# Performance work log

Measured on AMD Instinct MI355X. Metric: run time of the kernel, lower is better.

The kernel has to match this reference:

```python
import jax, jax.numpy as jnp
import numpy as np

DIM = 384
HEADS = 6
HEAD_DIM = 64
WIN = 14
SCALE = HEAD_DIM ** -0.5
EPS = 1e-5  # torch LayerNorm default


def setup_inputs() -> dict:
    key = jax.random.key(0)
    ks = jax.random.split(key, 8)
    w = lambda k, shape: jax.random.normal(k, shape, dtype=jnp.float32) * 0.02
    return {
        "x": jax.random.normal(ks[0], (1, 336, 336, DIM), dtype=jnp.float32),
        "qkv_w": w(ks[1], (DIM, 3 * DIM)),
        "qkv_b": jnp.zeros((3 * DIM,), jnp.float32),
        "proj_w": w(ks[2], (DIM, DIM)),
        "proj_b": jnp.zeros((DIM,), jnp.float32),
        "rel_pos_h": w(ks[3], (2 * WIN - 1, HEAD_DIM)),
        "rel_pos_w": w(ks[4], (2 * WIN - 1, HEAD_DIM)),
        "norm1_w": jnp.ones((DIM,), jnp.float32),
        "norm1_b": jnp.zeros((DIM,), jnp.float32),
        "norm2_w": jnp.ones((DIM,), jnp.float32),
        "norm2_b": jnp.zeros((DIM,), jnp.float32),
        "fc1_w": w(ks[5], (DIM, 4 * DIM)),
        "fc1_b": jnp.zeros((4 * DIM,), jnp.float32),
        "fc2_w": w(ks[6], (4 * DIM, DIM)),
        "fc2_b": jnp.zeros((DIM,), jnp.float32),
    }


def _layernorm(x, w, b):
    m = jnp.mean(x, axis=-1, keepdims=True)
    v = jnp.var(x, axis=-1, keepdims=True)
    return (x - m) / jnp.sqrt(v + EPS) * w + b


def _rel_table(rel_pos):
    coords = np.arange(WIN)[:, None] - np.arange(WIN)[None, :] + (WIN - 1)
    return rel_pos[coords]


def _block(x, qkv_w, qkv_b, proj_w, proj_b, rel_pos_h, rel_pos_w,
           norm1_w, norm1_b, norm2_w, norm2_b, fc1_w, fc1_b, fc2_w, fc2_b):
    B, H, W, C = x.shape
    shortcut = x
    x = _layernorm(x, norm1_w, norm1_b)

    nH, nW = H // WIN, W // WIN
    xw = x.reshape(B, nH, WIN, nW, WIN, C).transpose(0, 1, 3, 2, 4, 5)
    xw = xw.reshape(B * nH * nW, WIN * WIN, C)  # [Nw, 196, C]
    Nw, L = xw.shape[0], WIN * WIN

    # --- attention with decomposed rel-pos ---
    qkv = xw @ qkv_w + qkv_b                         # [Nw, 196, 3C]
    qkv = qkv.reshape(Nw, L, 3, HEADS, HEAD_DIM).transpose(2, 0, 3, 1, 4)
    q, k, v = qkv[0], qkv[1], qkv[2]                 # [Nw, h, 196, d]

    attn = jnp.einsum("bhqd,bhkd->bhqk", q * SCALE, k)  # [Nw, h, 196, 196]

    Rh = _rel_table(rel_pos_h)                       # [14, 14, d]
    Rw = _rel_table(rel_pos_w)
    r_q = q.reshape(Nw, HEADS, WIN, WIN, HEAD_DIM)
    rel_h = jnp.einsum("bnhwc,hkc->bnhwk", r_q, Rh)  # [Nw, h, 14, 14, 14]
    rel_w = jnp.einsum("bnhwc,wkc->bnhwk", r_q, Rw)
    attn = (attn.reshape(Nw, HEADS, WIN, WIN, WIN, WIN)
            + rel_h[..., :, None] + rel_w[..., None, :]).reshape(Nw, HEADS, L, L)

    attn = jax.nn.softmax(attn, axis=-1)
    out = jnp.einsum("bhqk,bhkd->bhqd", attn, v)     # [Nw, h, 196, d]
    out = out.transpose(0, 2, 1, 3).reshape(Nw, L, C)
    out = out @ proj_w + proj_b

    # --- window unpartition ---
    out = out.reshape(B, nH, nW, WIN, WIN, C).transpose(0, 1, 3, 2, 4, 5)
    out = out.reshape(B, H, W, C)

    x = shortcut + out
    h = _layernorm(x, norm2_w, norm2_b)
    h = jax.nn.gelu(h @ fc1_w + fc1_b, approximate=False) @ fc2_w + fc2_b
    return x + h


def reference(x, qkv_w, qkv_b, proj_w, proj_b, rel_pos_h, rel_pos_w,
              norm1_w, norm1_b, norm2_w, norm2_b, fc1_w, fc1_b, fc2_w, fc2_b):
    return _block(x, qkv_w, qkv_b, proj_w, proj_b, rel_pos_h, rel_pos_w,
                  norm1_w, norm1_b, norm2_w, norm2_b, fc1_w, fc1_b, fc2_w, fc2_b)
```

## Files before the change

kernel.cpp:

```cpp
#include <hip/hip_runtime.h>
#include <math.h>

#define TOKENS 112896
#define C      384
#define NQKV   1152
#define NFC    1536
#define HEADS  6
#define HD     64
#define WIN    14
#define L      196
#define NWS    24
#define SCALEF 0.125f

typedef unsigned int  u32;
typedef unsigned short u16;
typedef short short8 __attribute__((ext_vector_type(8)));
typedef float floatx4 __attribute__((ext_vector_type(4)));

__device__ __forceinline__ u16 f2bf(float f) {
  u32 u = __float_as_uint(f);
  u += 0x7FFFu + ((u >> 16) & 1u);
  return (u16)(u >> 16);
}

__device__ __forceinline__ float bf2f(u16 v) {
  return __uint_as_float((u32)v << 16);
}

__device__ __forceinline__ float gelu_f(float v) {
  float z = fabsf(v) * 0.70710678118654752f;
  float t = 1.0f / (1.0f + 0.3275911f * z);
  float poly = t * (0.254829592f + t * (-0.284496736f + t * (1.421413741f +
               t * (-1.453152027f + t * 1.061405429f))));
  float erfv = 1.0f - poly * __expf(-z * z);
  erfv = copysignf(erfv, v);
  return 0.5f * v * (1.0f + erfv);
}

__device__ __forceinline__ void async16(u16* lds, const u16* g) {
  __builtin_amdgcn_global_load_lds((const __attribute__((address_space(1))) void*)g,
                                   (__attribute__((address_space(3))) void*)lds,
                                   16, 0, 0);
}

__device__ __forceinline__ int win_to_tok(int r) {
  int n = r / L, l = r % L;
  int wh = n / NWS, ww = n % NWS;
  int ih = l / WIN, iw = l % WIN;
  return (wh * WIN + ih) * 336 + ww * WIN + iw;
}

__global__ __launch_bounds__(256) void conv_t_kernel(const float* __restrict__ in,
    u16* __restrict__ out, int K, int N)
{
  __shared__ u16 tile[32][33];
  const int kb = blockIdx.y * 32, nb = blockIdx.x * 32;
  const int tx = threadIdx.x & 31, ty = threadIdx.x >> 5;
#pragma unroll
  for (int i = 0; i < 4; i++) {
    int k = kb + ty + i * 8;
    tile[ty + i * 8][tx] = f2bf(in[(size_t)k * N + nb + tx]);
  }
  __syncthreads();
#pragma unroll
  for (int i = 0; i < 4; i++) {
    int n = nb + ty + i * 8;
    out[(size_t)n * K + kb + tx] = tile[tx][ty + i * 8];
  }
}

template<bool PERMUTE>
__global__ __launch_bounds__(128) void ln_kernel(const float* __restrict__ x,
    const float* __restrict__ w, const float* __restrict__ b,
    u16* __restrict__ out)
{
  const int t = blockIdx.x;
  const int tid = threadIdx.x;
  const float* xr = x + (size_t)t * C;
  float v0 = xr[tid], v1 = xr[tid + 128], v2 = xr[tid + 256];
  float s  = v0 + v1 + v2;
  float ss = v0 * v0 + v1 * v1 + v2 * v2;
#pragma unroll
  for (int off = 32; off > 0; off >>= 1) {
    s  += __shfl_down(s, off);
    ss += __shfl_down(ss, off);
  }
  __shared__ float red[4];
  if ((tid & 63) == 0) { red[(tid >> 6) * 2 + 0] = s; red[(tid >> 6) * 2 + 1] = ss; }
  __syncthreads();
  float S  = red[0] + red[2];
  float SS = red[1] + red[3];
  float mean = S * (1.0f / C);
  float var  = SS * (1.0f / C) - mean * mean;
  float rstd = rsqrtf(var + 1e-5f);
  size_t orow;
  if (PERMUTE) {
    int h_ = t / 336, w_ = t % 336;
    int wh = h_ / WIN, ih = h_ % WIN;
    int ww = w_ / WIN, iw = w_ % WIN;
    orow = (size_t)((wh * NWS + ww) * L + ih * WIN + iw);
  } else {
    orow = (size_t)t;
  }
  u16* op = out + orow * C;
  op[tid]       = f2bf((v0 - mean) * rstd * w[tid]       + b[tid]);
  op[tid + 128] = f2bf((v1 - mean) * rstd * w[tid + 128] + b[tid + 128]);
  op[tid + 256] = f2bf((v2 - mean) * rstd * w[tid + 256] + b[tid + 256]);
}

template<int MODE>
__global__ __launch_bounds__(256, 4) void gemm_bf16(
    const u16* __restrict__ A, const u16* __restrict__ Bt,
    const float* __restrict__ bias, const float* __restrict__ res,
    void* __restrict__ outv, int N, int K)
{
  __shared__ u16 As[2][128 * 32];
  __shared__ u16 Bs[2][128 * 32];
  const int tid = threadIdx.x;
  const int w = tid >> 6, l = tid & 63;

  const int nwg = gridDim.x * gridDim.y;
  int lin = blockIdx.y * gridDim.x + blockIdx.x;
  {
    int q8 = nwg >> 3, r8 = nwg & 7;
    int xcd = lin & 7, sub = lin >> 3;
    lin = (xcd < r8 ? xcd * (q8 + 1) : r8 * (q8 + 1) + (xcd - r8) * q8) + sub;
  }
  const int bx = lin % gridDim.x, by = lin / gridDim.x;
  const int bm = by * 128, bn = bx * 128;

  const int wm = (w >> 1) * 64, wn = (w & 1) * 64;
  const int lm = l & 15, quad = l >> 4;

  floatx4 acc[4][4] = {};

  const u16* Asrc[2]; const u16* Bsrc[2];
#pragma unroll
  for (int q = 0; q < 2; q++) {
    int t = q * 256 + tid;
    int r = t >> 2, gl = t & 3;
    int sg = gl ^ ((r >> 1) & 3);
    Asrc[q] = A  + (size_t)(bm + r) * K + sg * 8;
    Bsrc[q] = Bt + (size_t)(bn + r) * K + sg * 8;
  }
  u16* Ad[2]; u16* Bd[2];
#pragma unroll
  for (int q = 0; q < 2; q++) {
    Ad[q] = &As[0][(q * 256 + w * 64) * 8];
    Bd[q] = &Bs[0][(q * 256 + w * 64) * 8];
  }
  const int bufoff = 128 * 32;

  auto stage = [&](int buf, int kt) {
#pragma unroll
    for (int q = 0; q < 2; q++) {
      async16(Ad[q] + buf * bufoff, Asrc[q] + kt);
      async16(Bd[q] + buf * bufoff, Bsrc[q] + kt);
    }
  };

  const int xg = (quad ^ ((lm >> 1) & 3)) * 8;
  const u16* ard[4]; const u16* brd[4];
#pragma unroll
  for (int i = 0; i < 4; i++) {
    ard[i] = &As[0][(wm + i * 16 + lm) * 32 + xg];
    brd[i] = &Bs[0][(wn + i * 16 + lm) * 32 + xg];
  }

  const int nk = K >> 5;
  stage(0, 0);
  __syncthreads();

  for (int t = 0; t < nk; t++) {
    const int buf = t & 1;
    if (t + 1 < nk) stage(buf ^ 1, (t + 1) << 5);
    const int bo = buf * bufoff;
    short8 bfr[4];
#pragma unroll
    for (int j = 0; j < 4; j++) bfr[j] = *(const short8*)(brd[j] + bo);
#pragma unroll
    for (int i = 0; i < 4; i++) {
      short8 afr = *(const short8*)(ard[i] + bo);
#pragma unroll
      for (int j = 0; j < 4; j++)
        acc[i][j] = __builtin_amdgcn_mfma_f32_16x16x32_bf16(afr, bfr[j], acc[i][j], 0, 0, 0);
    }
    __syncthreads();
  }

  const int colbase = bn + wn + lm;
  float bb[4];
#pragma unroll
  for (int j = 0; j < 4; j++) bb[j] = bias[colbase + j * 16];

#pragma unroll
  for (int i = 0; i < 4; i++) {
#pragma unroll
    for (int reg = 0; reg < 4; reg++) {
      int row = bm + wm + i * 16 + quad * 4 + reg;
      size_t ro;
      if (MODE == 1) ro = (size_t)win_to_tok(row) * N;
      else           ro = (size_t)row * N;
#pragma unroll
      for (int j = 0; j < 4; j++) {
        float v = acc[i][j][reg] + bb[j];
        int col = colbase + j * 16;
        if (MODE == 0) {
          ((u16*)outv)[ro + col] = f2bf(v);
        } else if (MODE == 1) {
          ((float*)outv)[ro + col] = v + res[ro + col];
        } else if (MODE == 2) {
          ((u16*)outv)[ro + col] = f2bf(gelu_f(v));
        } else {
          ((float*)outv)[ro + col] = v + res[ro + col];
        }
      }
    }
  }
}

__global__ __launch_bounds__(256, 2) void attn_kernel(
    const u16* __restrict__ qkv,
    const float* __restrict__ relh, const float* __restrict__ relw,
    u16* __restrict__ out)
{
  __shared__ float Plds[4][512];
  __shared__ u16 rhlds[208 * 28];
  __shared__ u16 rwlds[208 * 28];
  __shared__ u16 Klds[32 * 64];
  __shared__ u16 Vtl[64 * 40];

  const int n = blockIdx.x / HEADS;
  const int h = blockIdx.x % HEADS;
  const int tid = threadIdx.x;
  const int w = tid >> 6;
  const int l = tid & 63;
  const int lm = l & 15;
  const int quad = l >> 4;
  const size_t base = (size_t)n * L;

  short8 qf[4][2];
#pragma unroll
  for (int i = 0; i < 4; i++) {
    int rt = w + 4 * i;
    if (rt <= 12) {
      int row = rt * 16 + lm; if (row > 195) row = 195;
      const u16* qp = qkv + (base + row) * NQKV + h * HD + quad * 8;
#pragma unroll
      for (int kf = 0; kf < 2; kf++)
        qf[i][kf] = *(const short8*)(qp + kf * 32);
    }
  }

  {
    short8 tf[2][2][2];
#pragma unroll
    for (int tab = 0; tab < 2; tab++) {
      const float* tp = tab ? relw : relh;
#pragma unroll
      for (int ct = 0; ct < 2; ct++) {
        int t = ct * 16 + lm;
#pragma unroll
        for (int kf = 0; kf < 2; kf++) {
          short8 v = {0, 0, 0, 0, 0, 0, 0, 0};
          if (t < 27) {
            const float* p = tp + t * HD + kf * 32 + quad * 8;
            float4 a = *(const float4*)p;
            float4 b = *(const float4*)(p + 4);
            v[0] = (short)f2bf(a.x); v[1] = (short)f2bf(a.y);
            v[2] = (short)f2bf(a.z); v[3] = (short)f2bf(a.w);
            v[4] = (short)f2bf(b.x); v[5] = (short)f2bf(b.y);
            v[6] = (short)f2bf(b.z); v[7] = (short)f2bf(b.w);
          }
          tf[tab][ct][kf] = v;
        }
      }
    }
#pragma unroll
    for (int i = 0; i < 4; i++) {
      int rt = w + 4 * i;
      if (rt > 12) continue;
#pragma unroll
      for (int tab = 0; tab < 2; tab++) {
        u16* dst = tab ? rwlds : rhlds;
#pragma unroll
        for (int ct = 0; ct < 2; ct++) {
          floatx4 acc = {};
          acc = __builtin_amdgcn_mfma_f32_16x16x32_bf16(qf[i][0], tf[tab][ct][0], acc, 0, 0, 0);
          acc = __builtin_amdgcn_mfma_f32_16x16x32_bf16(qf[i][1], tf[tab][ct][1], acc, 0, 0, 0);
          int t = ct * 16 + lm;
          if (t < 28) {
#pragma unroll
            for (int reg = 0; reg < 4; reg++) {
              int q = rt * 16 + quad * 4 + reg;
              dst[q * 28 + t] = f2bf(acc[reg]);
            }
          }
        }
      }
    }
  }

  floatx4 oacc[4][4] = {};
  float lsum[4][4] = {};

#pragma unroll 1
  for (int ks = 0; ks < 7; ks++) {
    __syncthreads();
    {
      int r = tid >> 3, g = tid & 7;
      int row = ks * 32 + r; if (row > 195) row = 195;
      uint4 kd = *(const uint4*)(qkv + (base + row) * NQKV + C + h * HD + g * 8);
      *(uint4*)&Klds[r * 64 + ((g ^ (r & 7)) * 8)] = kd;
    }
    {
      int r = tid & 31, seg = tid >> 5;
      int row = ks * 32 + r; if (row > 195) row = 195;
      uint4 vd = *(const uint4*)(qkv + (base + row) * NQKV + 2 * C + h * HD + seg * 8);
      union { uint4 u; u16 s[8]; } vv; vv.u = vd;
#pragma unroll
      for (int j = 0; j < 8; j++) Vtl[(seg * 8 + j) * 40 + r] = vv.s[j];
    }
    __syncthreads();

    short8 kfr[2][2];
#pragma unroll
    for (int ct = 0; ct < 2; ct++) {
      int krow = ct * 16 + lm;
#pragma unroll
      for (int kf = 0; kf < 2; kf++)
        kfr[ct][kf] = *(const short8*)&Klds[krow * 64 + (((kf * 4 + quad) ^ (krow & 7)) * 8)];
    }
    short8 vfr[4];
#pragma unroll
    for (int dt = 0; dt < 4; dt++)
      vfr[dt] = *(const short8*)&Vtl[(dt * 16 + lm) * 40 + quad * 8];

#pragma unroll
    for (int i = 0; i < 4; i++) {
      int rt = w + 4 * i;
      if (rt > 12) continue;
      floatx4 sc[2] = {};
#pragma unroll
      for (int ct = 0; ct < 2; ct++) {
        sc[ct] = __builtin_amdgcn_mfma_f32_16x16x32_bf16(qf[i][0], kfr[ct][0], sc[ct], 0, 0, 0);
        sc[ct] = __builtin_amdgcn_mfma_f32_16x16x32_bf16(qf[i][1], kfr[ct][1], sc[ct], 0, 0, 0);
      }
      float* Pw = Plds[w];
#pragma unroll
      for (int ct = 0; ct < 2; ct++) {
        int k = ks * 32 + ct * 16 + lm;
        int kh = (k * 293) >> 12;
        int kw2 = k - kh * 14;
        bool kval = (k < 196);
#pragma unroll
        for (int reg = 0; reg < 4; reg++) {
          int q = rt * 16 + quad * 4 + reg;
          int qh = (q * 293) >> 12;
          int qw = q - qh * 14;
          int th = qh - kh + 13; th = th < 0 ? 0 : th;
          int tw = qw - kw2 + 13;
          float bh = bf2f(rhlds[q * 28 + th]);
          float bw = bf2f(rwlds[q * 28 + tw]);
          float s = sc[ct][reg] * SCALEF + bh + bw;
          float p = kval ? __expf(s) : 0.0f;
          lsum[i][reg] += p;
          int prow = quad * 4 + reg;
          int col = ct * 16 + lm;
          Pw[prow * 32 + (((col >> 2) ^ (prow & 7)) * 4) + (col & 3)] = p;
        }
      }
      floatx4 pa = *(const floatx4*)&Pw[lm * 32 + (((2 * quad) ^ (lm & 7)) * 4)];
      floatx4 pb = *(const floatx4*)&Pw[lm * 32 + (((2 * quad + 1) ^ (lm & 7)) * 4)];
      short8 pfr;
#pragma unroll
      for (int j = 0; j < 4; j++) {
        pfr[j]     = (short)f2bf(pa[j]);
        pfr[4 + j] = (short)f2bf(pb[j]);
      }
#pragma unroll
      for (int dt = 0; dt < 4; dt++)
        oacc[i][dt] = __builtin_amdgcn_mfma_f32_16x16x32_bf16(pfr, vfr[dt], oacc[i][dt], 0, 0, 0);
    }
  }

#pragma unroll
  for (int i = 0; i < 4; i++) {
    int rt = w + 4 * i;
    if (rt > 12) continue;
#pragma unroll
    for (int reg = 0; reg < 4; reg++) {
      float v = lsum[i][reg];
      v += __shfl_xor(v, 1);
      v += __shfl_xor(v, 2);
      v += __shfl_xor(v, 4);
      v += __shfl_xor(v, 8);
      float inv = 1.0f / v;
      int row = rt * 16 + quad * 4 + reg;
      if (row < 196) {
        u16* op = out + (base + row) * C + h * HD + lm;
#pragma unroll
        for (int dt = 0; dt < 4; dt++) op[dt * 16] = f2bf(oacc[i][dt][reg] * inv);
      }
    }
  }
}

extern "C" void kernel_launch(void* const* d_in, const int* in_sizes, int n_in,
                              void* d_out, int out_size, void* d_ws, size_t ws_size,
                              hipStream_t stream)
{
  const float* x      = (const float*)d_in[0];
  const float* qkv_w  = (const float*)d_in[1];
  const float* qkv_b  = (const float*)d_in[2];
  const float* proj_w = (const float*)d_in[3];
  const float* proj_b = (const float*)d_in[4];
  const float* rel_h  = (const float*)d_in[5];
  const float* rel_w  = (const float*)d_in[6];
  const float* n1w    = (const float*)d_in[7];
  const float* n1b    = (const float*)d_in[8];
  const float* n2w    = (const float*)d_in[9];
  const float* n2b    = (const float*)d_in[10];
  const float* fc1_w  = (const float*)d_in[11];
  const float* fc1_b  = (const float*)d_in[12];
  const float* fc2_w  = (const float*)d_in[13];
  const float* fc2_b  = (const float*)d_in[14];

  u16*  W0 = (u16*)d_ws;
  u16*  W1 = (u16*)((char*)d_ws + 86704128);
  float* W2 = (float*)((char*)d_ws + 86704128 + 346816512);
  u16*  WT = (u16*)((char*)d_ws + 86704128 + 346816512 + 173408256);
  u16* qkv_wT  = WT;
  u16* proj_wT = qkv_wT + 442368;
  u16* fc1_wT  = proj_wT + 147456;
  u16* fc2_wT  = fc1_wT + 589824;

  conv_t_kernel<<<dim3(NQKV / 32, C / 32), 256, 0, stream>>>(qkv_w, qkv_wT, C, NQKV);
  conv_t_kernel<<<dim3(C / 32, C / 32), 256, 0, stream>>>(proj_w, proj_wT, C, C);
  conv_t_kernel<<<dim3(NFC / 32, C / 32), 256, 0, stream>>>(fc1_w, fc1_wT, C, NFC);
  conv_t_kernel<<<dim3(C / 32, NFC / 32), 256, 0, stream>>>(fc2_w, fc2_wT, NFC, C);

  ln_kernel<true><<<TOKENS, 128, 0, stream>>>(x, n1w, n1b, W0);
  gemm_bf16<0><<<dim3(NQKV / 128, TOKENS / 128), 256, 0, stream>>>(
      W0, qkv_wT, qkv_b, nullptr, W1, NQKV, C);
  attn_kernel<<<576 * HEADS, 256, 0, stream>>>(W1, rel_h, rel_w, W0);
  gemm_bf16<1><<<dim3(C / 128, TOKENS / 128), 256, 0, stream>>>(
      W0, proj_wT, proj_b, x, W2, C, C);
  ln_kernel<false><<<TOKENS, 128, 0, stream>>>(W2, n2w, n2b, W0);
  gemm_bf16<2><<<dim3(NFC / 128, TOKENS / 128), 256, 0, stream>>>(
      W0, fc1_wT, fc1_b, nullptr, W1, NFC, C);
  gemm_bf16<3><<<dim3(C / 128, TOKENS / 128), 256, 0, stream>>>(
      W1, fc2_wT, fc2_b, W2, (float*)d_out, C, NFC);
}
```

Before: 1.386 ms.

## Transpose MFMA operands for vectorized epilogue stores and unroll GEMM k-loop by two

```diff
diff --git a/kernel.cpp b/kernel.cpp
--- a/kernel.cpp
+++ b/kernel.cpp
@@ -25,6 +25,12 @@
 
 __device__ __forceinline__ float bf2f(u16 v) {
   return __uint_as_float((u32)v << 16);
+}
+
+__device__ __forceinline__ u32 pk2bf(float lo, float hi) {
+  u32 r;
+  asm("v_cvt_pk_bf16_f32 %0, %1, %2" : "=v"(r) : "v"(lo), "v"(hi));
+  return r;
 }
 
 __device__ __forceinline__ float gelu_f(float v) {
@@ -134,14 +140,14 @@
 
   floatx4 acc[4][4] = {};
 
-  const u16* Asrc[2]; const u16* Bsrc[2];
+  u32 aofs[2], bofs[2];
 #pragma unroll
   for (int q = 0; q < 2; q++) {
     int t = q * 256 + tid;
     int r = t >> 2, gl = t & 3;
     int sg = gl ^ ((r >> 1) & 3);
-    Asrc[q] = A  + (size_t)(bm + r) * K + sg * 8;
-    Bsrc[q] = Bt + (size_t)(bn + r) * K + sg * 8;
+    aofs[q] = (u32)((bm + r) * K + sg * 8);
+    bofs[q] = (u32)((bn + r) * K + sg * 8);
   }
   u16* Ad[2]; u16* Bd[2];
 #pragma unroll
@@ -149,15 +155,17 @@
     Ad[q] = &As[0][(q * 256 + w * 64) * 8];
     Bd[q] = &Bs[0][(q * 256 + w * 64) * 8];
   }
-  const int bufoff = 128 * 32;
-
-  auto stage = [&](int buf, int kt) {
-#pragma unroll
-    for (int q = 0; q < 2; q++) {
-      async16(Ad[q] + buf * bufoff, Asrc[q] + kt);
-      async16(Bd[q] + buf * bufoff, Bsrc[q] + kt);
-    }
-  };
+
+#define STAGE(buf, kt)                                         \
+  {                                                            \
+    const u16* Ap = A  + (kt);                                 \
+    const u16* Bp = Bt + (kt);                                 \
+    _Pragma("unroll")                                          \
+    for (int q = 0; q < 2; q++) {                              \
+      async16(Ad[q] + (buf) * 4096, Ap + aofs[q]);             \
+      async16(Bd[q] + (buf) * 4096, Bp + bofs[q]);             \
+    }                                                          \
+  }
 
   const int xg = (quad ^ ((lm >> 1) & 3)) * 8;
   const u16* ard[4]; const u16* brd[4];
@@ -167,53 +175,66 @@
     brd[i] = &Bs[0][(wn + i * 16 + lm) * 32 + xg];
   }
 
+#define COMPUTE(BO)                                                         \
+  {                                                                         \
+    short8 bfr[4];                                                          \
+    _Pragma("unroll")                                                       \
+    for (int i2 = 0; i2 < 4; i2++)                                          \
+      bfr[i2] = *(const short8*)(brd[i2] + (BO));                           \
+    _Pragma("unroll")                                                       \
+    for (int j2 = 0; j2 < 4; j2++) {                                        \
+      short8 afr = *(const short8*)(ard[j2] + (BO));                        \
+      _Pragma("unroll")                                                     \
+      for (int i2 = 0; i2 < 4; i2++)                                        \
+        acc[i2][j2] = __builtin_amdgcn_mfma_f32_16x16x32_bf16(              \
+            bfr[i2], afr, acc[i2][j2], 0, 0, 0);                            \
+    }                                                                       \
+  }
+
   const int nk = K >> 5;
-  stage(0, 0);
+  STAGE(0, 0);
   __syncthreads();
 
-  for (int t = 0; t < nk; t++) {
-    const int buf = t & 1;
-    if (t + 1 < nk) stage(buf ^ 1, (t + 1) << 5);
-    const int bo = buf * bufoff;
-    short8 bfr[4];
-#pragma unroll
-    for (int j = 0; j < 4; j++) bfr[j] = *(const short8*)(brd[j] + bo);
+  for (int t = 0; t < nk; t += 2) {
+    STAGE(1, (t + 1) << 5);
+    COMPUTE(0);
+    __syncthreads();
+    if (t + 2 < nk) STAGE(0, (t + 2) << 5);
+    COMPUTE(4096);
+    __syncthreads();
+  }
+#undef STAGE
+#undef COMPUTE
+
+  float4 bb[4];
+#pragma unroll
+  for (int i = 0; i < 4; i++)
+    bb[i] = *(const float4*)&bias[bn + wn + i * 16 + quad * 4];
+
+#pragma unroll
+  for (int j = 0; j < 4; j++) {
+    int m = bm + wm + j * 16 + lm;
+    size_t ro;
+    if (MODE == 1) ro = (size_t)win_to_tok(m) * N;
+    else           ro = (size_t)m * N;
 #pragma unroll
     for (int i = 0; i < 4; i++) {
-      short8 afr = *(const short8*)(ard[i] + bo);
-#pragma unroll
-      for (int j = 0; j < 4; j++)
-        acc[i][j] = __builtin_amdgcn_mfma_f32_16x16x32_bf16(afr, bfr[j], acc[i][j], 0, 0, 0);
-    }
-    __syncthreads();
-  }
-
-  const int colbase = bn + wn + lm;
-  float bb[4];
-#pragma unroll
-  for (int j = 0; j < 4; j++) bb[j] = bias[colbase + j * 16];
-
-#pragma unroll
-  for (int i = 0; i < 4; i++) {
-#pragma unroll
-    for (int reg = 0; reg < 4; reg++) {
-      int row = bm + wm + i * 16 + quad * 4 + reg;
-      size_t ro;
-      if (MODE == 1) ro = (size_t)win_to_tok(row) * N;
-      else           ro = (size_t)row * N;
-#pragma unroll
-      for (int j = 0; j < 4; j++) {
-        float v = acc[i][j][reg] + bb[j];
-        int col = colbase + j * 16;
-        if (MODE == 0) {
-          ((u16*)outv)[ro + col] = f2bf(v);
-        } else if (MODE == 1) {
-          ((float*)outv)[ro + col] = v + res[ro + col];
-        } else if (MODE == 2) {
-          ((u16*)outv)[ro + col] = f2bf(gelu_f(v));
-        } else {
-          ((float*)outv)[ro + col] = v + res[ro + col];
-        }
+      int n0 = bn + wn + i * 16 + quad * 4;
+      float v0 = acc[i][j][0] + bb[i].x;
+      float v1 = acc[i][j][1] + bb[i].y;
+      float v2 = acc[i][j][2] + bb[i].z;
+      float v3 = acc[i][j][3] + bb[i].w;
+      if (MODE == 0) {
+        uint2 st = make_uint2(pk2bf(v0, v1), pk2bf(v2, v3));
+        *(uint2*)((u16*)outv + ro + n0) = st;
+      } else if (MODE == 2) {
+        uint2 st = make_uint2(pk2bf(gelu_f(v0), gelu_f(v1)),
+                              pk2bf(gelu_f(v2), gelu_f(v3)));
+        *(uint2*)((u16*)outv + ro + n0) = st;
+      } else {
+        float4 r4 = *(const float4*)&res[ro + n0];
+        float4 o = make_float4(v0 + r4.x, v1 + r4.y, v2 + r4.z, v3 + r4.w);
+        *(float4*)&((float*)outv)[ro + n0] = o;
       }
     }
   }
```

Result: slower. 1.415 ms (+2.1%).
